# Kernel tuning notes

Hardware: AMD Instinct MI355X
Metric: run time of the kernel (lower is better)

The kernel has to match this reference:

```python
import jax, jax.numpy as jnp
import numpy as np

D_MODEL = 1024
D_HIDDEN = 4096
D_VOCAB = 32000
N_CTX = 2048
N_LAYERS = 8


def setup_inputs() -> dict:
    key = jax.random.key(0)
    ks = jax.random.split(key, 10)
    # scale params by 1/sqrt(fan_in) so softmax/logits are numerically sane
    s = 1.0 / np.sqrt(D_MODEL)
    sh = 1.0 / np.sqrt(D_HIDDEN)
    return {
        "tokens": jax.random.randint(ks[0], (N_CTX,), 0, D_VOCAB),
        "tok_emb": jax.random.normal(ks[1], (D_VOCAB, D_MODEL), jnp.float32) * s,
        "pos_emb": jax.random.normal(ks[2], (N_CTX, D_MODEL), jnp.float32) * s,
        "wqk": jax.random.normal(ks[3], (N_LAYERS, D_MODEL, D_MODEL), jnp.float32) * s,
        "wov": jax.random.normal(ks[4], (N_LAYERS, D_MODEL, D_MODEL), jnp.float32) * s,
        "w_up": jax.random.normal(ks[5], (N_LAYERS, D_HIDDEN, D_MODEL), jnp.float32) * s,
        "b_up": jax.random.normal(ks[6], (N_LAYERS, D_HIDDEN), jnp.float32) * 0.01,
        "w_down": jax.random.normal(ks[7], (N_LAYERS, D_MODEL, D_HIDDEN), jnp.float32) * sh,
        "b_down": jax.random.normal(ks[8], (N_LAYERS, D_MODEL), jnp.float32) * 0.01,
    }


def reference(tokens, tok_emb, pos_emb, wqk, wov, w_up, b_up, w_down, b_down):
    n = tokens.shape[0]
    # token + positional embedding  -> [n, d_model]
    x = tok_emb[tokens] + pos_emb[:n]
    # causal additive mask: -inf strictly above the diagonal
    idx = jnp.arange(n)
    mask = jnp.where(idx[None, :] > idx[:, None], -jnp.inf, 0.0).astype(x.dtype)
    for l in range(wqk.shape[0]):
        # MLP branch: relu(x W_up^T + b_up) W_down^T + b_down
        h = jnp.maximum(x @ w_up[l].T + b_up[l], 0.0) @ w_down[l].T + b_down[l]
        # attention branch: softmax(x Wqk x^T + M) x Wov
        scores = (x @ wqk[l]) @ x.T + mask          # [n, n]
        attn = jax.nn.softmax(scores, axis=-1) @ x @ wov[l]
        x = x + h + attn                             # parallel residual
    # tied unembedding -> logits [n, d_vocab]
    return x @ tok_emb.T
```

## Files before the change

kernel.cpp:

```cpp
#include <hip/hip_runtime.h>
#include <hip/hip_bf16.h>
#include <stdint.h>

#define DM 1024
#define DH 4096
#define DV 32000
#define NC 2048
#define NL 8

typedef float f32x4_t __attribute__((ext_vector_type(4)));
typedef __bf16 bf16x8_t __attribute__((ext_vector_type(8)));
typedef unsigned short u16x4_t __attribute__((ext_vector_type(4)));
typedef unsigned short u16x8_t __attribute__((ext_vector_type(8)));

typedef __attribute__((address_space(1))) void as1_void;
typedef __attribute__((address_space(3))) void as3_void;

__device__ __forceinline__ unsigned short f2bf(float f) {
  unsigned int u = __builtin_bit_cast(unsigned int, f);
  u += 0x7fffu + ((u >> 16) & 1u);
  return (unsigned short)(u >> 16);
}

__device__ __forceinline__ void gload_lds16(const void* g, void* l) {
  __builtin_amdgcn_global_load_lds((as1_void*)(void*)g, (as3_void*)l, 16, 0, 0);
}

__device__ __forceinline__ void cast_tail8(const float* __restrict__ src,
                                           unsigned short* __restrict__ dst,
                                           size_t n, int cidx, int tid) {
  for (size_t i = (size_t)cidx * 2048 + (size_t)tid * 8; i < n;
       i += (size_t)512 * 2048) {
    const float4 a = *reinterpret_cast<const float4*>(src + i);
    const float4 b = *reinterpret_cast<const float4*>(src + i + 4);
    u16x8_t v;
    v[0] = f2bf(a.x); v[1] = f2bf(a.y); v[2] = f2bf(a.z); v[3] = f2bf(a.w);
    v[4] = f2bf(b.x); v[5] = f2bf(b.y); v[6] = f2bf(b.z); v[7] = f2bf(b.w);
    *reinterpret_cast<u16x8_t*>(dst + i) = v;
  }
}

template <int BNT, bool B_FP32, bool SPLIT, bool CAUSAL, bool CAUSAL_K,
          bool HAS_BIAS, bool RELU, bool OUT_BF16>
__device__ __forceinline__ void gemm_body(
    unsigned short* As, unsigned short* Bs, const unsigned short* __restrict__ A,
    const void* __restrict__ Bt, const float* __restrict__ bias,
    void* __restrict__ Cout, int M, int N, int lda, int Ks, int bx, int by,
    int koff, int zslice) {
  constexpr int BK = 64;
  constexpr int BN = BNT;
  constexpr int CPTA = 4;
  constexpr int CPTB = (BN * BK) / 2048;
  constexpr int NF = BN / 32;
  const int t = threadIdx.x;
  const int lane = t & 63;
  const int wid = t >> 6;
  const int wr = wid >> 1, wc = wid & 1;
  const int row0 = by * 128;
  const int col0 = bx * BN;

  if constexpr (CAUSAL) {
    if (col0 > row0 + 127) return;
  }

  int Kend = Ks;
  if constexpr (CAUSAL_K) {
    const int need = row0 + 128 - koff;
    Kend = need <= 0 ? 0 : (need >= Ks ? Ks : ((need + BK - 1) & ~(BK - 1)));
    if constexpr (SPLIT) {
      if (Kend <= 0) return;
    }
  }

  f32x4_t acc[4][NF];
#pragma unroll
  for (int m = 0; m < 4; m++)
#pragma unroll
    for (int n = 0; n < NF; n++) acc[m][n] = (f32x4_t){0.f, 0.f, 0.f, 0.f};

  for (int kt = 0; kt < Kend; kt += BK) {
    __syncthreads();
#pragma unroll
    for (int i = 0; i < CPTA; i++) {
      const int c = i * 256 + t;
      const int r = c >> 3;
      const int ko = ((c & 7) ^ (r & 7)) * 8;
      const unsigned short* g = A + (size_t)(row0 + r) * lda + koff + kt + ko;
      unsigned short* l = &As[(size_t)(i * 256 + wid * 64) * 8];
      gload_lds16(g, l);
    }
    if constexpr (B_FP32) {
      const float* Bf = (const float*)Bt;
#pragma unroll
      for (int i = 0; i < CPTB; i++) {
        const int c = i * 256 + t;
        const int r = c >> 3;
        const int ko = ((c & 7) ^ (r & 7)) * 8;
        const float* g = Bf + (size_t)(col0 + r) * lda + koff + kt + ko;
        const float4 f0 = *reinterpret_cast<const float4*>(g);
        const float4 f1 = *reinterpret_cast<const float4*>(g + 4);
        u16x8_t v;
        v[0] = f2bf(f0.x); v[1] = f2bf(f0.y); v[2] = f2bf(f0.z); v[3] = f2bf(f0.w);
        v[4] = f2bf(f1.x); v[5] = f2bf(f1.y); v[6] = f2bf(f1.z); v[7] = f2bf(f1.w);
        *reinterpret_cast<u16x8_t*>(&Bs[(size_t)c * 8]) = v;
      }
    } else {
      const unsigned short* Bu = (const unsigned short*)Bt;
#pragma unroll
      for (int i = 0; i < CPTB; i++) {
        const int c = i * 256 + t;
        const int r = c >> 3;
        const int ko = ((c & 7) ^ (r & 7)) * 8;
        const unsigned short* g = Bu + (size_t)(col0 + r) * lda + koff + kt + ko;
        unsigned short* l = &Bs[(size_t)(i * 256 + wid * 64) * 8];
        gload_lds16(g, l);
      }
    }
    __syncthreads();

#pragma unroll
    for (int kk = 0; kk < 2; kk++) {
      bf16x8_t av[4], bv[NF];
#pragma unroll
      for (int m = 0; m < 4; m++) {
        const int arow = wr * 64 + m * 16 + (lane & 15);
        const int akc = (kk * 4 + (lane >> 4)) ^ (arow & 7);
        av[m] = __builtin_bit_cast(
            bf16x8_t, *reinterpret_cast<const u16x8_t*>(&As[arow * BK + akc * 8]));
      }
#pragma unroll
      for (int n = 0; n < NF; n++) {
        const int brow = wc * (BN / 2) + n * 16 + (lane & 15);
        const int bkc = (kk * 4 + (lane >> 4)) ^ (brow & 7);
        bv[n] = __builtin_bit_cast(
            bf16x8_t, *reinterpret_cast<const u16x8_t*>(&Bs[brow * BK + bkc * 8]));
      }
#pragma unroll
      for (int m = 0; m < 4; m++)
#pragma unroll
        for (int n = 0; n < NF; n++)
          acc[m][n] = __builtin_amdgcn_mfma_f32_16x16x32_bf16(av[m], bv[n],
                                                              acc[m][n], 0, 0, 0);
    }
  }

#pragma unroll
  for (int m = 0; m < 4; m++) {
    const int rbase = row0 + wr * 64 + m * 16 + (lane >> 4) * 4;
#pragma unroll
    for (int n = 0; n < NF; n++) {
      const int col = col0 + wc * (BN / 2) + n * 16 + (lane & 15);
      if constexpr (SPLIT) {
        float* out = (float*)Cout + (size_t)zslice * M * N;
#pragma unroll
        for (int j = 0; j < 4; j++)
          out[(size_t)(rbase + j) * N + col] = acc[m][n][j];
      } else {
        float bval = 0.0f;
        if constexpr (HAS_BIAS) bval = bias[col];
#pragma unroll
        for (int j = 0; j < 4; j++) {
          float v = acc[m][n][j];
          if constexpr (HAS_BIAS) v += bval;
          if constexpr (RELU) v = fmaxf(v, 0.0f);
          const size_t idx = (size_t)(rbase + j) * N + col;
          if constexpr (OUT_BF16)
            ((unsigned short*)Cout)[idx] = f2bf(v);
          else
            __builtin_nontemporal_store(v, (float*)Cout + idx);
        }
      }
    }
  }
}

__device__ __forceinline__ void super_decode(int idx, int gy, int& bx, int& by) {
  const int s = idx >> 4;
  const int u = idx & 15;
  const int sgy = gy >> 2;
  const int sx = s / sgy;
  const int sy = s - sx * sgy;
  bx = sx * 4 + (u & 3);
  by = sy * 4 + (u >> 2);
}

template <int BNT, bool B_FP32, bool SPLIT, bool CAUSAL, bool CAUSAL_K,
          bool HAS_BIAS, bool RELU, bool OUT_BF16>
__global__ __launch_bounds__(256) void gemm_nt(
    const unsigned short* __restrict__ A, const void* __restrict__ Bt,
    const float* __restrict__ bias, void* __restrict__ Cout, int M, int N,
    int lda, int Ks) {
  __shared__ __attribute__((aligned(16))) unsigned short As[128 * 64];
  __shared__ __attribute__((aligned(16))) unsigned short Bs[BNT * 64];
  const int gx = gridDim.x, gy = gridDim.y;
  const int nwg = gx * gy;
  const int orig = blockIdx.y * gx + blockIdx.x;
  const int qq = nwg >> 3, rr = nwg & 7;
  const int xc = orig & 7, ii = orig >> 3;
  const int wgid = (xc < rr ? xc * (qq + 1) : rr * (qq + 1) + (xc - rr) * qq) + ii;
  int bx, by;
  super_decode(wgid, gy, bx, by);
  gemm_body<BNT, B_FP32, SPLIT, CAUSAL, CAUSAL_K, HAS_BIAS, RELU, OUT_BF16>(
      As, Bs, A, Bt, bias, Cout, M, N, lda, Ks, bx, by,
      SPLIT ? blockIdx.z * Ks : 0, blockIdx.z);
}

__global__ __launch_bounds__(256) void fused_up_q(
    const unsigned short* __restrict__ xb, const unsigned short* __restrict__ wupB,
    const float* __restrict__ bup, unsigned short* __restrict__ h1,
    const unsigned short* __restrict__ wqkT, float* __restrict__ qpool,
    const float* __restrict__ c0s, unsigned short* __restrict__ c0d, size_t c0n,
    const float* __restrict__ c1s, unsigned short* __restrict__ c1d, size_t c1n) {
  __shared__ __attribute__((aligned(16))) unsigned short As[128 * 64];
  __shared__ __attribute__((aligned(16))) unsigned short Bs[64 * 64];
  const int orig = blockIdx.x;
  const int xc = orig & 7, ii = orig >> 3;
  int bx, by;
  if (ii < 128) {
    const int idx = xc * 128 + ii;
    super_decode(idx, 16, bx, by);
    gemm_body<64, false, false, false, false, true, true, true>(
        As, Bs, xb, wupB, bup, h1, NC, DH, DM, DM, bx, by, 0, 0);
  } else if (ii < 192) {
    const int idx = xc * 64 + (ii - 128);
    const int z = idx >> 8;
    super_decode(idx & 255, 16, bx, by);
    gemm_body<64, false, true, false, false, false, false, false>(
        As, Bs, xb, wqkT, nullptr, qpool, NC, DM, DM, DM / 2, bx, by,
        z * (DM / 2), z);
  } else {
    const int cidx = xc * 64 + (ii - 192);
    cast_tail8(c0s, c0d, c0n, cidx, threadIdx.x);
    cast_tail8(c1s, c1d, c1n, cidx, threadIdx.x);
  }
}

__global__ __launch_bounds__(256) void fused_down_rq(
    const unsigned short* __restrict__ h1, const unsigned short* __restrict__ wdownB,
    float* __restrict__ dpart, const float* __restrict__ qpool,
    unsigned short* __restrict__ qb,
    const float* __restrict__ c0s, unsigned short* __restrict__ c0d, size_t c0n,
    const float* __restrict__ c1s, unsigned short* __restrict__ c1d, size_t c1n) {
  __shared__ __attribute__((aligned(16))) unsigned short As[128 * 64];
  __shared__ __attribute__((aligned(16))) unsigned short Bs[64 * 64];
  const int orig = blockIdx.x;
  const int xc = orig & 7, ii = orig >> 3;
  if (ii < 128) {
    const int idx = xc * 128 + ii;
    const int z = idx >> 8;
    int bx, by;
    super_decode(idx & 255, 16, bx, by);
    gemm_body<64, false, true, false, false, false, false, false>(
        As, Bs, h1, wdownB, nullptr, dpart, NC, DM, DH, DH / 4, bx, by,
        z * (DH / 4), z);
  } else if (ii < 384) {
    const int ridx = xc * 256 + (ii - 128);
    const size_t nMD = (size_t)NC * DM;
    const size_t i = ((size_t)ridx * 256 + threadIdx.x) * 4;
    if (i < nMD) {
      float4 v = *reinterpret_cast<const float4*>(qpool + i);
      const float4 w = *reinterpret_cast<const float4*>(qpool + nMD + i);
      v.x += w.x; v.y += w.y; v.z += w.z; v.w += w.w;
      u16x4_t o;
      o[0] = f2bf(v.x); o[1] = f2bf(v.y); o[2] = f2bf(v.z); o[3] = f2bf(v.w);
      *reinterpret_cast<u16x4_t*>(qb + i) = o;
    }
  } else {
    const int cidx = xc * 64 + (ii - 384);
    cast_tail8(c0s, c0d, c0n, cidx, threadIdx.x);
    cast_tail8(c1s, c1d, c1n, cidx, threadIdx.x);
  }
}

__global__ __launch_bounds__(256) void cast3_f32_bf16(
    const float* __restrict__ in0, unsigned short* __restrict__ out0, size_t n0,
    const float* __restrict__ in1, unsigned short* __restrict__ out1, size_t n1,
    const float* __restrict__ in2, unsigned short* __restrict__ out2, size_t n2,
    int gper) {
  const int seg = blockIdx.x / gper;
  const int lb = blockIdx.x - seg * gper;
  const float* in = seg == 0 ? in0 : (seg == 1 ? in1 : in2);
  unsigned short* out = seg == 0 ? out0 : (seg == 1 ? out1 : out2);
  const size_t n = seg == 0 ? n0 : (seg == 1 ? n1 : n2);
  const size_t stride = (size_t)gper * 256 * 8;
  for (size_t i = ((size_t)lb * 256 + threadIdx.x) * 8; i < n; i += stride) {
    const float4 a = *reinterpret_cast<const float4*>(in + i);
    const float4 b = *reinterpret_cast<const float4*>(in + i + 4);
    u16x8_t v;
    v[0] = f2bf(a.x); v[1] = f2bf(a.y); v[2] = f2bf(a.z); v[3] = f2bf(a.w);
    v[4] = f2bf(b.x); v[5] = f2bf(b.y); v[6] = f2bf(b.z); v[7] = f2bf(b.w);
    *reinterpret_cast<u16x8_t*>(out + i) = v;
  }
}

__global__ __launch_bounds__(256) void embed_kernel(
    const int* __restrict__ tokens, const float* __restrict__ tok_emb,
    const float* __restrict__ pos_emb, float* __restrict__ x,
    unsigned short* __restrict__ xb) {
  const int i = blockIdx.x;
  const int tok = tokens[i];
  const float* te = tok_emb + (size_t)tok * DM;
  const float* pe = pos_emb + (size_t)i * DM;
  float* xr = x + (size_t)i * DM;
  unsigned short* xbr = xb + (size_t)i * DM;
  const int j = threadIdx.x * 4;
  const float4 a = *reinterpret_cast<const float4*>(te + j);
  const float4 b = *reinterpret_cast<const float4*>(pe + j);
  float4 v;
  v.x = a.x + b.x; v.y = a.y + b.y; v.z = a.z + b.z; v.w = a.w + b.w;
  *reinterpret_cast<float4*>(xr + j) = v;
  u16x4_t o;
  o[0] = f2bf(v.x); o[1] = f2bf(v.y); o[2] = f2bf(v.z); o[3] = f2bf(v.w);
  *reinterpret_cast<u16x4_t*>(xbr + j) = o;
}

__global__ void transpose_cast_dual(const float* __restrict__ in0,
                                    unsigned short* __restrict__ out0,
                                    const float* __restrict__ in1,
                                    unsigned short* __restrict__ out1, int R,
                                    int C, int ZSPLIT) {
  __shared__ float tile[32][33];
  const int z = blockIdx.z;
  const float* in = (z < ZSPLIT) ? in0 : in1;
  unsigned short* out = (z < ZSPLIT) ? out0 : out1;
  const int zl = (z < ZSPLIT) ? z : z - ZSPLIT;
  const size_t lo = (size_t)zl * R * C;
  const int x = blockIdx.x * 32 + threadIdx.x;
#pragma unroll
  for (int i = threadIdx.y; i < 32; i += 8) {
    const int y = blockIdx.y * 32 + i;
    tile[i][threadIdx.x] = in[lo + (size_t)y * C + x];
  }
  __syncthreads();
  const int ox = blockIdx.y * 32 + threadIdx.x;
#pragma unroll
  for (int i = threadIdx.y; i < 32; i += 8) {
    const int oy = blockIdx.x * 32 + i;
    out[lo + (size_t)oy * R + ox] = f2bf(tile[threadIdx.x][i]);
  }
}

__global__ void transpose_u16(const unsigned short* __restrict__ in,
                              unsigned short* __restrict__ out, int R, int C) {
  __shared__ unsigned short tile[32][33];
  const int x = blockIdx.x * 32 + threadIdx.x;
#pragma unroll
  for (int i = threadIdx.y; i < 32; i += 8) {
    const int y = blockIdx.y * 32 + i;
    tile[i][threadIdx.x] = in[(size_t)y * C + x];
  }
  __syncthreads();
  const int ox = blockIdx.y * 32 + threadIdx.x;
#pragma unroll
  for (int i = threadIdx.y; i < 32; i += 8) {
    const int oy = blockIdx.x * 32 + i;
    out[(size_t)oy * R + ox] = tile[threadIdx.x][i];
  }
}

__global__ __launch_bounds__(256) void softmax_split2(
    const float* __restrict__ p0, const float* __restrict__ p1,
    unsigned short* __restrict__ P, int n) {
  __shared__ float srow[NC];
  __shared__ float sred[4];
  const int i = blockIdx.x;
  const int valid = i + 1;
  const int wlimit = (i & ~127) + 128;
  const int t = threadIdx.x;
  const int wid = t >> 6, lane = t & 63;
  const size_t ro = (size_t)i * n;
  for (int j = t; j < valid; j += 256) srow[j] = p0[ro + j] + p1[ro + j];
  __syncthreads();

  float m = -3.0e38f;
  for (int j = t; j < valid; j += 256) m = fmaxf(m, srow[j]);
#pragma unroll
  for (int o = 32; o > 0; o >>= 1) m = fmaxf(m, __shfl_xor(m, o, 64));
  if (lane == 0) sred[wid] = m;
  __syncthreads();
  m = fmaxf(fmaxf(sred[0], sred[1]), fmaxf(sred[2], sred[3]));
  __syncthreads();

  float s = 0.f;
  for (int j = t; j < valid; j += 256) s += __expf(srow[j] - m);
#pragma unroll
  for (int o = 32; o > 0; o >>= 1) s += __shfl_xor(s, o, 64);
  if (lane == 0) sred[wid] = s;
  __syncthreads();
  s = sred[0] + sred[1] + sred[2] + sred[3];
  const float inv = 1.0f / s;

  unsigned short* prow = P + ro;
  for (int j = t; j < wlimit; j += 256)
    prow[j] = (j < valid) ? f2bf(__expf(srow[j] - m) * inv) : (unsigned short)0;
}

__global__ __launch_bounds__(256) void softmax_causal(
    const float* __restrict__ S, unsigned short* __restrict__ P, int n) {
  __shared__ float srow[NC];
  __shared__ float sred[4];
  const int i = blockIdx.x;
  const int valid = i + 1;
  const int t = threadIdx.x;
  const int wid = t >> 6, lane = t & 63;
  const size_t ro = (size_t)i * n;
  for (int j = t; j < valid; j += 256) srow[j] = S[ro + j];
  __syncthreads();
  float m = -3.0e38f;
  for (int j = t; j < valid; j += 256) m = fmaxf(m, srow[j]);
#pragma unroll
  for (int o = 32; o > 0; o >>= 1) m = fmaxf(m, __shfl_xor(m, o, 64));
  if (lane == 0) sred[wid] = m;
  __syncthreads();
  m = fmaxf(fmaxf(sred[0], sred[1]), fmaxf(sred[2], sred[3]));
  __syncthreads();
  float s = 0.f;
  for (int j = t; j < valid; j += 256) s += __expf(srow[j] - m);
#pragma unroll
  for (int o = 32; o > 0; o >>= 1) s += __shfl_xor(s, o, 64);
  if (lane == 0) sred[wid] = s;
  __syncthreads();
  s = sred[0] + sred[1] + sred[2] + sred[3];
  const float inv = 1.0f / s;
  unsigned short* prow = P + ro;
  for (int j = t; j < n; j += 256)
    prow[j] = (j < valid) ? f2bf(__expf(srow[j] - m) * inv) : (unsigned short)0;
}

template <int NS>
__global__ __launch_bounds__(256) void reduce_to_bf16(
    const float* __restrict__ part, unsigned short* __restrict__ out, size_t n,
    size_t stride) {
  const size_t i = ((size_t)blockIdx.x * 256 + threadIdx.x) * 4;
  if (i >= n) return;
  float4 v = *reinterpret_cast<const float4*>(part + i);
#pragma unroll
  for (int s = 1; s < NS; s++) {
    const float4 w = *reinterpret_cast<const float4*>(part + (size_t)s * stride + i);
    v.x += w.x; v.y += w.y; v.z += w.z; v.w += w.w;
  }
  u16x4_t o;
  o[0] = f2bf(v.x); o[1] = f2bf(v.y); o[2] = f2bf(v.z); o[3] = f2bf(v.w);
  *reinterpret_cast<u16x4_t*>(out + i) = o;
}

__global__ __launch_bounds__(256) void reduce_pv_causal(
    const float* __restrict__ part, unsigned short* __restrict__ out, size_t n,
    size_t stride) {
  const size_t i = ((size_t)blockIdx.x * 256 + threadIdx.x) * 4;
  if (i >= n) return;
  const int row = (int)(i >> 10);
  const int nsl = (row >> 9) + 1;
  float4 v = *reinterpret_cast<const float4*>(part + i);
  for (int s = 1; s < nsl; s++) {
    const float4 w = *reinterpret_cast<const float4*>(part + (size_t)s * stride + i);
    v.x += w.x; v.y += w.y; v.z += w.z; v.w += w.w;
  }
  u16x4_t o;
  o[0] = f2bf(v.x); o[1] = f2bf(v.y); o[2] = f2bf(v.z); o[3] = f2bf(v.w);
  *reinterpret_cast<u16x4_t*>(out + i) = o;
}

__global__ __launch_bounds__(256) void residual_tiled(
    float* __restrict__ x, unsigned short* __restrict__ xb,
    unsigned short* __restrict__ xT, const float* __restrict__ dp,
    const float* __restrict__ op, const float* __restrict__ bd) {
  __shared__ unsigned short tile[32][33];
  const int tx = threadIdx.x;
  const int ty = threadIdx.y;
  const int col0 = blockIdx.x * 32;
  const int row0 = blockIdx.y * 32;
  const size_t n = (size_t)NC * DM;
  const int row = row0 + ty;
  const int col = col0 + tx * 4;
  const size_t idx = (size_t)row * DM + col;

  float4 v = *reinterpret_cast<const float4*>(x + idx);
  const float4 b = *reinterpret_cast<const float4*>(bd + col);
  v.x += b.x; v.y += b.y; v.z += b.z; v.w += b.w;
#pragma unroll
  for (int s = 0; s < 4; s++) {
    const float4 w = *reinterpret_cast<const float4*>(dp + (size_t)s * n + idx);
    v.x += w.x; v.y += w.y; v.z += w.z; v.w += w.w;
  }
#pragma unroll
  for (int s = 0; s < 2; s++) {
    const float4 w = *reinterpret_cast<const float4*>(op + (size_t)s * n + idx);
    v.x += w.x; v.y += w.y; v.z += w.z; v.w += w.w;
  }
  *reinterpret_cast<float4*>(x + idx) = v;
  u16x4_t o;
  o[0] = f2bf(v.x); o[1] = f2bf(v.y); o[2] = f2bf(v.z); o[3] = f2bf(v.w);
  *reinterpret_cast<u16x4_t*>(xb + idx) = o;
  tile[ty][tx * 4 + 0] = o[0];
  tile[ty][tx * 4 + 1] = o[1];
  tile[ty][tx * 4 + 2] = o[2];
  tile[ty][tx * 4 + 3] = o[3];
  __syncthreads();

  const int t = ty * 8 + tx;
  const int wc = t >> 5;
  const int wr = t & 31;
#pragma unroll
  for (int j = 0; j < 4; j++) {
    const int c = wc + j * 8;
    xT[(size_t)(col0 + c) * NC + row0 + wr] = tile[wr][c];
  }
}

__global__ __launch_bounds__(256) void residual_kernel(
    float* __restrict__ x, const float* __restrict__ hd,
    const float* __restrict__ attn, unsigned short* __restrict__ xb, int n) {
  const int idx = blockIdx.x * 256 + threadIdx.x;
  if (idx < n) {
    const float v = x[idx] + hd[idx] + attn[idx];
    x[idx] = v;
    xb[idx] = f2bf(v);
  }
}

extern "C" void kernel_launch(void* const* d_in, const int* in_sizes, int n_in,
                              void* d_out, int out_size, void* d_ws,
                              size_t ws_size, hipStream_t stream) {
  const int* tokens = (const int*)d_in[0];
  const float* tok_emb = (const float*)d_in[1];
  const float* pos_emb = (const float*)d_in[2];
  const float* wqk = (const float*)d_in[3];
  const float* wov = (const float*)d_in[4];
  const float* w_up = (const float*)d_in[5];
  const float* b_up = (const float*)d_in[6];
  const float* w_down = (const float*)d_in[7];
  const float* b_down = (const float*)d_in[8];
  float* logits = (float*)d_out;

  uint8_t* base = (uint8_t*)d_ws;
  size_t used = 0;
  auto alloc = [&](size_t bytes) -> void* {
    const size_t ab = (bytes + 255) & ~(size_t)255;
    if (used + ab > ws_size) return (void*)0;
    void* r = base + used;
    used += ab;
    return r;
  };

  float* x = (float*)alloc((size_t)NC * DM * 4);
  unsigned short* xb = (unsigned short*)alloc((size_t)NC * DM * 2);
  unsigned short* h1 = (unsigned short*)alloc((size_t)NC * DH * 2);
  unsigned short* qb = (unsigned short*)alloc((size_t)NC * DM * 2);
  unsigned short* Pb = (unsigned short*)alloc((size_t)NC * NC * 2);
  unsigned short* xT = (unsigned short*)alloc((size_t)NC * DM * 2);
  unsigned short* ab = (unsigned short*)alloc((size_t)NC * DM * 2);
  unsigned short* wqkT = (unsigned short*)alloc((size_t)NL * DM * DM * 2);
  unsigned short* wovT = (unsigned short*)alloc((size_t)NL * DM * DM * 2);
  float* hd = (float*)alloc((size_t)NC * DM * 4);
  float* attn = (float*)alloc((size_t)NC * DM * 4);
  float* scores = (float*)alloc((size_t)NC * NC * 4);
  float* dpart = (float*)alloc((size_t)4 * NC * DM * 4);
  float* opart = (float*)alloc((size_t)2 * NC * DM * 4);
  float* pool = (float*)alloc((size_t)2 * NC * NC * 4);
  unsigned short* wupB = (unsigned short*)alloc((size_t)NL * DH * DM * 2);
  unsigned short* wdownB = (unsigned short*)alloc((size_t)NL * DM * DH * 2);
  unsigned short* tokB = (unsigned short*)alloc((size_t)DV * DM * 2);

  const bool split_en = (dpart && opart && pool);
  const bool have_wbf = (wupB && wdownB);
  const bool have_tok = (tokB != 0);
  const bool fused_en = split_en && have_wbf;

  const dim3 tb(32, 8);
  transpose_cast_dual<<<dim3(DM / 32, DM / 32, 2 * NL), tb, 0, stream>>>(
      wqk, wqkT, wov, wovT, DM, DM, NL);
  if (fused_en) {
    cast3_f32_bf16<<<2 * 1024, 256, 0, stream>>>(
        w_up, wupB, (size_t)DH * DM, w_down, wdownB, (size_t)DM * DH,
        nullptr, nullptr, 0, 1024);
  } else if (have_wbf && have_tok) {
    cast3_f32_bf16<<<3 * 2048, 256, 0, stream>>>(
        w_up, wupB, (size_t)NL * DH * DM, w_down, wdownB, (size_t)NL * DM * DH,
        tok_emb, tokB, (size_t)DV * DM, 2048);
  }
  embed_kernel<<<NC, 256, 0, stream>>>(tokens, tok_emb, pos_emb, x, xb);
  transpose_u16<<<dim3(DM / 32, NC / 32), tb, 0, stream>>>(xb, xT, NC, DM);

  const size_t nMD = (size_t)NC * DM;
  const size_t tokQ = (size_t)DV * DM / (2 * NL);

  for (int l = 0; l < NL; l++) {
    if (fused_en) {
      const bool nw = (l + 1 < NL);
      const float* u0s = nw ? w_up + (size_t)(l + 1) * DH * DM : nullptr;
      unsigned short* u0d = nw ? wupB + (size_t)(l + 1) * DH * DM : nullptr;
      const size_t u0n = nw ? (size_t)DH * DM : 0;
      const float* d0s = nw ? w_down + (size_t)(l + 1) * DM * DH : nullptr;
      unsigned short* d0d = nw ? wdownB + (size_t)(l + 1) * DM * DH : nullptr;
      const size_t d0n = nw ? (size_t)DM * DH : 0;
      const float* t0s = have_tok ? tok_emb + (size_t)l * 2 * tokQ : nullptr;
      unsigned short* t0d = have_tok ? tokB + (size_t)l * 2 * tokQ : nullptr;
      const float* t1s = have_tok ? tok_emb + (size_t)l * 2 * tokQ + tokQ : nullptr;
      unsigned short* t1d = have_tok ? tokB + (size_t)l * 2 * tokQ + tokQ : nullptr;
      const size_t tn = have_tok ? tokQ : 0;

      fused_up_q<<<2048, 256, 0, stream>>>(
          xb, wupB + (size_t)l * DH * DM, b_up + (size_t)l * DH, h1,
          wqkT + (size_t)l * DM * DM, pool, u0s, u0d, u0n, t0s, t0d, tn);
      fused_down_rq<<<3584, 256, 0, stream>>>(
          h1, wdownB + (size_t)l * DM * DH, dpart, pool, qb, d0s, d0d, d0n,
          t1s, t1d, tn);
    } else {
      gemm_nt<64, true, false, false, false, true, true, true>
          <<<dim3(DH / 64, NC / 128), 256, 0, stream>>>(
              xb, w_up + (size_t)l * DH * DM, b_up + (size_t)l * DH, h1, NC, DH, DM, DM);
      gemm_nt<64, true, false, false, false, true, false, false>
          <<<dim3(DM / 64, NC / 128), 256, 0, stream>>>(
              h1, w_down + (size_t)l * DM * DH, b_down + (size_t)l * DM, hd, NC, DM, DH, DH);
      gemm_nt<64, false, false, false, false, false, false, true>
          <<<dim3(DM / 64, NC / 128), 256, 0, stream>>>(
              xb, wqkT + (size_t)l * DM * DM, nullptr, qb, NC, DM, DM, DM);
    }

    if (split_en) {
      gemm_nt<64, false, true, true, false, false, false, false>
          <<<dim3(NC / 64, NC / 128, 2), 256, 0, stream>>>(
              qb, xb, nullptr, pool, NC, NC, DM, DM / 2);
      softmax_split2<<<NC, 256, 0, stream>>>(pool, pool + (size_t)NC * NC, Pb, NC);
    } else {
      gemm_nt<64, false, false, true, false, false, false, false>
          <<<dim3(NC / 64, NC / 128), 256, 0, stream>>>(
              qb, xb, nullptr, scores, NC, NC, DM, DM);
      softmax_causal<<<NC, 256, 0, stream>>>(scores, Pb, NC);
    }

    if (!split_en)
      transpose_u16<<<dim3(DM / 32, NC / 32), tb, 0, stream>>>(xb, xT, NC, DM);

    if (split_en) {
      gemm_nt<64, false, true, false, true, false, false, false>
          <<<dim3(DM / 64, NC / 128, 4), 256, 0, stream>>>(
              Pb, xT, nullptr, pool, NC, DM, NC, NC / 4);
      reduce_pv_causal<<<(nMD / 4 + 255) / 256, 256, 0, stream>>>(pool, ab, nMD, nMD);
    } else {
      gemm_nt<64, false, false, false, true, false, false, true>
          <<<dim3(DM / 64, NC / 128), 256, 0, stream>>>(
              Pb, xT, nullptr, ab, NC, DM, NC, NC);
    }

    if (split_en) {
      gemm_nt<64, false, true, false, false, false, false, false>
          <<<dim3(DM / 64, NC / 128, 2), 256, 0, stream>>>(
              ab, wovT + (size_t)l * DM * DM, nullptr, opart, NC, DM, DM, DM / 2);
      residual_tiled<<<dim3(DM / 32, NC / 32), dim3(8, 32), 0, stream>>>(
          x, xb, xT, dpart, opart, b_down + (size_t)l * DM);
    } else {
      gemm_nt<64, false, false, false, false, false, false, false>
          <<<dim3(DM / 64, NC / 128), 256, 0, stream>>>(
              ab, wovT + (size_t)l * DM * DM, nullptr, attn, NC, DM, DM, DM);
      residual_kernel<<<(int)(nMD / 256), 256, 0, stream>>>(x, hd, attn, xb, (int)nMD);
    }
  }

  if (fused_en && have_tok)
    gemm_nt<64, false, false, false, false, false, false, false>
        <<<dim3(DV / 64, NC / 128), 256, 0, stream>>>(
            xb, tokB, nullptr, logits, NC, DV, DM, DM);
  else if (have_tok)
    gemm_nt<64, false, false, false, false, false, false, false>
        <<<dim3(DV / 64, NC / 128), 256, 0, stream>>>(
            xb, tokB, nullptr, logits, NC, DV, DM, DM);
  else
    gemm_nt<64, true, false, false, false, false, false, false>
        <<<dim3(DV / 64, NC / 128), 256, 0, stream>>>(
            xb, tok_emb, nullptr, logits, NC, DV, DM, DM);
}
```

Before: 1.355 ms.

## Fuse QK scores into down-proj launch and OV GEMM with residual epilogue

In the fused path, the Wqk projection now writes bf16 directly without split-K, which removes the separate q-pool reduction. The QK^T score GEMM (split-K by 2) moves into the down-projection launch, replacing that reduction work, so one kernel launch goes away. A new GEMM kernel computes attn@Wov without split-K and applies the residual update (x, bias, down partials) in its epilogue, writing x, xb and xT. This replaces the OV split GEMM plus the separate residual kernel. The cost is less parallelism for the Q and OV GEMMs and uncoalesced column-wise xT stores in the epilogue.

```diff
diff --git a/kernel.cpp b/kernel.cpp
--- a/kernel.cpp
+++ b/kernel.cpp
@@ -205,10 +205,112 @@
       SPLIT ? blockIdx.z * Ks : 0, blockIdx.z);
 }
 
+__global__ __launch_bounds__(256) void gemm_ov_res(
+    const unsigned short* __restrict__ A, const unsigned short* __restrict__ Bt,
+    float* __restrict__ x, unsigned short* __restrict__ xb,
+    unsigned short* __restrict__ xT, const float* __restrict__ dp,
+    const float* __restrict__ bd) {
+  __shared__ __attribute__((aligned(16))) unsigned short As[128 * 64];
+  __shared__ __attribute__((aligned(16))) unsigned short Bs[64 * 64];
+  const int gx = gridDim.x, gy = gridDim.y;
+  const int nwg = gx * gy;
+  const int orig = blockIdx.y * gx + blockIdx.x;
+  const int qq = nwg >> 3, rr = nwg & 7;
+  const int xc = orig & 7, ii = orig >> 3;
+  const int wgid = (xc < rr ? xc * (qq + 1) : rr * (qq + 1) + (xc - rr) * qq) + ii;
+  int bx, by;
+  super_decode(wgid, gy, bx, by);
+
+  const int t = threadIdx.x;
+  const int lane = t & 63;
+  const int wid = t >> 6;
+  const int wr = wid >> 1, wc = wid & 1;
+  const int row0 = by * 128;
+  const int col0 = bx * 64;
+
+  f32x4_t acc[4][2];
+#pragma unroll
+  for (int m = 0; m < 4; m++)
+#pragma unroll
+    for (int n = 0; n < 2; n++) acc[m][n] = (f32x4_t){0.f, 0.f, 0.f, 0.f};
+
+  for (int kt = 0; kt < DM; kt += 64) {
+    __syncthreads();
+#pragma unroll
+    for (int i = 0; i < 4; i++) {
+      const int c = i * 256 + t;
+      const int r = c >> 3;
+      const int ko = ((c & 7) ^ (r & 7)) * 8;
+      const unsigned short* g = A + (size_t)(row0 + r) * DM + kt + ko;
+      unsigned short* l = &As[(size_t)(i * 256 + wid * 64) * 8];
+      gload_lds16(g, l);
+    }
+#pragma unroll
+    for (int i = 0; i < 2; i++) {
+      const int c = i * 256 + t;
+      const int r = c >> 3;
+      const int ko = ((c & 7) ^ (r & 7)) * 8;
+      const unsigned short* g = Bt + (size_t)(col0 + r) * DM + kt + ko;
+      unsigned short* l = &Bs[(size_t)(i * 256 + wid * 64) * 8];
+      gload_lds16(g, l);
+    }
+    __syncthreads();
+
+#pragma unroll
+    for (int kk = 0; kk < 2; kk++) {
+      bf16x8_t av[4], bv[2];
+#pragma unroll
+      for (int m = 0; m < 4; m++) {
+        const int arow = wr * 64 + m * 16 + (lane & 15);
+        const int akc = (kk * 4 + (lane >> 4)) ^ (arow & 7);
+        av[m] = __builtin_bit_cast(
+            bf16x8_t, *reinterpret_cast<const u16x8_t*>(&As[arow * 64 + akc * 8]));
+      }
+#pragma unroll
+      for (int n = 0; n < 2; n++) {
+        const int brow = wc * 32 + n * 16 + (lane & 15);
+        const int bkc = (kk * 4 + (lane >> 4)) ^ (brow & 7);
+        bv[n] = __builtin_bit_cast(
+            bf16x8_t, *reinterpret_cast<const u16x8_t*>(&Bs[brow * 64 + bkc * 8]));
+      }
+#pragma unroll
+      for (int m = 0; m < 4; m++)
+#pragma unroll
+        for (int n = 0; n < 2; n++)
+          acc[m][n] = __builtin_amdgcn_mfma_f32_16x16x32_bf16(av[m], bv[n],
+                                                              acc[m][n], 0, 0, 0);
+    }
+  }
+
+  const size_t nMD = (size_t)NC * DM;
+#pragma unroll
+  for (int m = 0; m < 4; m++) {
+    const int rbase = row0 + wr * 64 + m * 16 + (lane >> 4) * 4;
+#pragma unroll
+    for (int n = 0; n < 2; n++) {
+      const int col = col0 + wc * 32 + n * 16 + (lane & 15);
+      const float bval = bd[col];
+      u16x4_t ot;
+#pragma unroll
+      for (int j = 0; j < 4; j++) {
+        const size_t idx = (size_t)(rbase + j) * DM + col;
+        float v = acc[m][n][j] + x[idx] + bval;
+#pragma unroll
+        for (int s = 0; s < 4; s++) v += dp[(size_t)s * nMD + idx];
+        x[idx] = v;
+        const unsigned short o = f2bf(v);
+        xb[idx] = o;
+        ot[j] = o;
+      }
+      *reinterpret_cast<u16x4_t*>(&xT[(size_t)col * NC + rbase]) = ot;
+    }
+  }
+}
+
 __global__ __launch_bounds__(256) void fused_up_q(
     const unsigned short* __restrict__ xb, const unsigned short* __restrict__ wupB,
     const float* __restrict__ bup, unsigned short* __restrict__ h1,
-    const unsigned short* __restrict__ wqkT, float* __restrict__ qpool,
+    const unsigned short* __restrict__ wqkT, unsigned short* __restrict__ qb,
     const float* __restrict__ c0s, unsigned short* __restrict__ c0d, size_t c0n,
     const float* __restrict__ c1s, unsigned short* __restrict__ c1d, size_t c1n) {
   __shared__ __attribute__((aligned(16))) unsigned short As[128 * 64];
@@ -221,24 +323,22 @@
     super_decode(idx, 16, bx, by);
     gemm_body<64, false, false, false, false, true, true, true>(
         As, Bs, xb, wupB, bup, h1, NC, DH, DM, DM, bx, by, 0, 0);
-  } else if (ii < 192) {
-    const int idx = xc * 64 + (ii - 128);
-    const int z = idx >> 8;
-    super_decode(idx & 255, 16, bx, by);
-    gemm_body<64, false, true, false, false, false, false, false>(
-        As, Bs, xb, wqkT, nullptr, qpool, NC, DM, DM, DM / 2, bx, by,
-        z * (DM / 2), z);
+  } else if (ii < 160) {
+    const int idx = xc * 32 + (ii - 128);
+    super_decode(idx, 16, bx, by);
+    gemm_body<64, false, false, false, false, false, false, true>(
+        As, Bs, xb, wqkT, nullptr, qb, NC, DM, DM, DM, bx, by, 0, 0);
   } else {
-    const int cidx = xc * 64 + (ii - 192);
+    const int cidx = xc * 64 + (ii - 160);
     cast_tail8(c0s, c0d, c0n, cidx, threadIdx.x);
     cast_tail8(c1s, c1d, c1n, cidx, threadIdx.x);
   }
 }
 
-__global__ __launch_bounds__(256) void fused_down_rq(
+__global__ __launch_bounds__(256) void fused_down_sc(
     const unsigned short* __restrict__ h1, const unsigned short* __restrict__ wdownB,
-    float* __restrict__ dpart, const float* __restrict__ qpool,
-    unsigned short* __restrict__ qb,
+    float* __restrict__ dpart, const unsigned short* __restrict__ qb,
+    const unsigned short* __restrict__ xbv, float* __restrict__ spool,
     const float* __restrict__ c0s, unsigned short* __restrict__ c0d, size_t c0n,
     const float* __restrict__ c1s, unsigned short* __restrict__ c1d, size_t c1n) {
   __shared__ __attribute__((aligned(16))) unsigned short As[128 * 64];
@@ -253,20 +353,16 @@
     gemm_body<64, false, true, false, false, false, false, false>(
         As, Bs, h1, wdownB, nullptr, dpart, NC, DM, DH, DH / 4, bx, by,
         z * (DH / 4), z);
-  } else if (ii < 384) {
-    const int ridx = xc * 256 + (ii - 128);
-    const size_t nMD = (size_t)NC * DM;
-    const size_t i = ((size_t)ridx * 256 + threadIdx.x) * 4;
-    if (i < nMD) {
-      float4 v = *reinterpret_cast<const float4*>(qpool + i);
-      const float4 w = *reinterpret_cast<const float4*>(qpool + nMD + i);
-      v.x += w.x; v.y += w.y; v.z += w.z; v.w += w.w;
-      u16x4_t o;
-      o[0] = f2bf(v.x); o[1] = f2bf(v.y); o[2] = f2bf(v.z); o[3] = f2bf(v.w);
-      *reinterpret_cast<u16x4_t*>(qb + i) = o;
-    }
+  } else if (ii < 256) {
+    const int idx = xc * 128 + (ii - 128);
+    const int z = idx >> 9;
+    int bx, by;
+    super_decode(idx & 511, 16, bx, by);
+    gemm_body<64, false, true, true, false, false, false, false>(
+        As, Bs, qb, xbv, nullptr, spool, NC, NC, DM, DM / 2, bx, by,
+        z * (DM / 2), z);
   } else {
-    const int cidx = xc * 64 + (ii - 384);
+    const int cidx = xc * 64 + (ii - 256);
     cast_tail8(c0s, c0d, c0n, cidx, threadIdx.x);
     cast_tail8(c1s, c1d, c1n, cidx, threadIdx.x);
   }
@@ -427,23 +523,6 @@
     prow[j] = (j < valid) ? f2bf(__expf(srow[j] - m) * inv) : (unsigned short)0;
 }
 
-template <int NS>
-__global__ __launch_bounds__(256) void reduce_to_bf16(
-    const float* __restrict__ part, unsigned short* __restrict__ out, size_t n,
-    size_t stride) {
-  const size_t i = ((size_t)blockIdx.x * 256 + threadIdx.x) * 4;
-  if (i >= n) return;
-  float4 v = *reinterpret_cast<const float4*>(part + i);
-#pragma unroll
-  for (int s = 1; s < NS; s++) {
-    const float4 w = *reinterpret_cast<const float4*>(part + (size_t)s * stride + i);
-    v.x += w.x; v.y += w.y; v.z += w.z; v.w += w.w;
-  }
-  u16x4_t o;
-  o[0] = f2bf(v.x); o[1] = f2bf(v.y); o[2] = f2bf(v.z); o[3] = f2bf(v.w);
-  *reinterpret_cast<u16x4_t*>(out + i) = o;
-}
-
 __global__ __launch_bounds__(256) void reduce_pv_causal(
     const float* __restrict__ part, unsigned short* __restrict__ out, size_t n,
     size_t stride) {
@@ -600,12 +679,20 @@
       unsigned short* t1d = have_tok ? tokB + (size_t)l * 2 * tokQ + tokQ : nullptr;
       const size_t tn = have_tok ? tokQ : 0;
 
-      fused_up_q<<<2048, 256, 0, stream>>>(
+      fused_up_q<<<1792, 256, 0, stream>>>(
           xb, wupB + (size_t)l * DH * DM, b_up + (size_t)l * DH, h1,
-          wqkT + (size_t)l * DM * DM, pool, u0s, u0d, u0n, t0s, t0d, tn);
-      fused_down_rq<<<3584, 256, 0, stream>>>(
-          h1, wdownB + (size_t)l * DM * DH, dpart, pool, qb, d0s, d0d, d0n,
-          t1s, t1d, tn);
+          wqkT + (size_t)l * DM * DM, qb, u0s, u0d, u0n, t0s, t0d, tn);
+      fused_down_sc<<<2560, 256, 0, stream>>>(
+          h1, wdownB + (size_t)l * DM * DH, dpart, qb, xb, pool, d0s, d0d,
+          d0n, t1s, t1d, tn);
+      softmax_split2<<<NC, 256, 0, stream>>>(pool, pool + (size_t)NC * NC, Pb, NC);
+      gemm_nt<64, false, true, false, true, false, false, false>
+          <<<dim3(DM / 64, NC / 128, 4), 256, 0, stream>>>(
+              Pb, xT, nullptr, pool, NC, DM, NC, NC / 4);
+      reduce_pv_causal<<<(nMD / 4 + 255) / 256, 256, 0, stream>>>(pool, ab, nMD, nMD);
+      gemm_ov_res<<<dim3(DM / 64, NC / 128), 256, 0, stream>>>(
+          ab, wovT + (size_t)l * DM * DM, x, xb, xT, dpart,
+          b_down + (size_t)l * DM);
     } else {
       gemm_nt<64, true, false, false, false, true, true, true>
           <<<dim3(DH / 64, NC / 128), 256, 0, stream>>>(
@@ -616,53 +703,39 @@
       gemm_nt<64, false, false, false, false, false, false, true>
           <<<dim3(DM / 64, NC / 128), 256, 0, stream>>>(
               xb, wqkT + (size_t)l * DM * DM, nullptr, qb, NC, DM, DM, DM);
-    }
-
-    if (split_en) {
-      gemm_nt<64, false, true, true, false, false, false, false>
-          <<<dim3(NC / 64, NC / 128, 2), 256, 0, stream>>>(
-              qb, xb, nullptr, pool, NC, NC, DM, DM / 2);
-      softmax_split2<<<NC, 256, 0, stream>>>(pool, pool + (size_t)NC * NC, Pb, NC);
-    } else {
-      gemm_nt<64, false, false, true, false, false, false, false>
-          <<<dim3(NC / 64, NC / 128), 256, 0, stream>>>(
-              qb, xb, nullptr, scores, NC, NC, DM, DM);
-      softmax_causal<<<NC, 256, 0, stream>>>(scores, Pb, NC);
-    }
-
-    if (!split_en)
-      transpose_u16<<<dim3(DM / 32, NC / 32), tb, 0, stream>>>(xb, xT, NC, DM);
-
-    if (split_en) {
-      gemm_nt<64, false, true, false, true, false, false, false>
-          <<<dim3(DM / 64, NC / 128, 4), 256, 0, stream>>>(
-              Pb, xT, nullptr, pool, NC, DM, NC, NC / 4);
-      reduce_pv_causal<<<(nMD / 4 + 255) / 256, 256, 0, stream>>>(pool, ab, nMD, nMD);
-    } else {
-      gemm_nt<64, false, false, false, true, false, false, true>
-          <<<dim3(DM / 64, NC / 128), 256, 0, stream>>>(
-              Pb, xT, nullptr, ab, NC, DM, NC, NC);
-    }
-
-    if (split_en) {
-      gemm_nt<64, false, true, false, false, false, false, false>
-          <<<dim3(DM / 64, NC / 128, 2), 256, 0, stream>>>(
-              ab, wovT + (size_t)l * DM * DM, nullptr, opart, NC, DM, DM, DM / 2);
-      residual_tiled<<<dim3(DM / 32, NC / 32), dim3(8, 32), 0, stream>>>(
-          x, xb, xT, dpart, opart, b_down + (size_t)l * DM);
-    } else {
-      gemm_nt<64, false, false, false, false, false, false, false>
-          <<<dim3(DM / 64, NC / 128), 256, 0, stream>>>(
-              ab, wovT + (size_t)l * DM * DM, nullptr, attn, NC, DM, DM, DM);
-      residual_kernel<<<(int)(nMD / 256), 256, 0, stream>>>(x, hd, attn, xb, (int)nMD);
-    }
-  }
-
-  if (fused_en && have_tok)
-    gemm_nt<64, false, false, false, false, false, false, false>
-        <<<dim3(DV / 64, NC / 128), 256, 0, stream>>>(
-            xb, tokB, nullptr, logits, NC, DV, DM, DM);
-  else if (have_tok)
+
+      if (split_en) {
+        gemm_nt<64, false, true, true, false, false, false, false>
+            <<<dim3(NC / 64, NC / 128, 2), 256, 0, stream>>>(
+                qb, xb, nullptr, pool, NC, NC, DM, DM / 2);
+        softmax_split2<<<NC, 256, 0, stream>>>(pool, pool + (size_t)NC * NC, Pb, NC);
+        gemm_nt<64, false, true, false, true, false, false, false>
+            <<<dim3(DM / 64, NC / 128, 4), 256, 0, stream>>>(
+                Pb, xT, nullptr, pool, NC, DM, NC, NC / 4);
+        reduce_pv_causal<<<(nMD / 4 + 255) / 256, 256, 0, stream>>>(pool, ab, nMD, nMD);
+        gemm_nt<64, false, true, false, false, false, false, false>
+            <<<dim3(DM / 64, NC / 128, 2), 256, 0, stream>>>(
+                ab, wovT + (size_t)l * DM * DM, nullptr, opart, NC, DM, DM, DM / 2);
+        residual_tiled<<<dim3(DM / 32, NC / 32), dim3(8, 32), 0, stream>>>(
+            x, xb, xT, dpart, opart, b_down + (size_t)l * DM);
+      } else {
+        gemm_nt<64, false, false, true, false, false, false, false>
+            <<<dim3(NC / 64, NC / 128), 256, 0, stream>>>(
+                qb, xb, nullptr, scores, NC, NC, DM, DM);
+        softmax_causal<<<NC, 256, 0, stream>>>(scores, Pb, NC);
+        transpose_u16<<<dim3(DM / 32, NC / 32), tb, 0, stream>>>(xb, xT, NC, DM);
+        gemm_nt<64, false, false, false, true, false, false, true>
+            <<<dim3(DM / 64, NC / 128), 256, 0, stream>>>(
+                Pb, xT, nullptr, ab, NC, DM, NC, NC);
+        gemm_nt<64, false, false, false, false, false, false, false>
+            <<<dim3(DM / 64, NC / 128), 256, 0, stream>>>(
+                ab, wovT + (size_t)l * DM * DM, nullptr, attn, NC, DM, DM, DM);
+        residual_kernel<<<(int)(nMD / 256), 256, 0, stream>>>(x, hd, attn, xb, (int)nMD);
+      }
+    }
+  }
+
+  if (have_tok && (fused_en || have_wbf))
     gemm_nt<64, false, false, false, false, false, false, false>
         <<<dim3(DV / 64, NC / 128), 256, 0, stream>>>(
             xb, tokB, nullptr, logits, NC, DV, DM, DM);
```

Result: faster. 1.288 ms (-4.9%).
